# Kernel optimization log

Measured on AMD Instinct MI355X. Metric: run time of the kernel, lower is better.

Reference implementation:

```python
import jax, jax.numpy as jnp
from jax import lax
import numpy as np

B, N, NPOINTS, DOWN_NUM, K = 4, 4096, 4096, 1024, 16
EPS = 1e-5


def setup_inputs() -> dict:
    key = jax.random.key(0)
    ks = jax.random.split(key, 8)
    w = lambda k, s: jax.random.normal(k, s, jnp.float32) * 0.05
    return {
        "x": jax.random.normal(ks[0], (B, 3, N), jnp.float32),
        "w_in": w(ks[1], (8, 3)), "b_in": jnp.zeros((8,), jnp.float32),
        "w1": w(ks[2], (32, 16)), "g1w": jnp.ones((32,), jnp.float32), "g1b": jnp.zeros((32,), jnp.float32),
        "w2": w(ks[3], (64, 64)), "g2w": jnp.ones((64,), jnp.float32), "g2b": jnp.zeros((64,), jnp.float32),
        "w3": w(ks[4], (64, 128)), "g3w": jnp.ones((64,), jnp.float32), "g3b": jnp.zeros((64,), jnp.float32),
        "w4": w(ks[5], (128, 128)), "g4w": jnp.ones((128,), jnp.float32), "g4b": jnp.zeros((128,), jnp.float32),
    }


def _knn_idx(coor_k, coor_q, k):
    # coor_*: (B,3,N) -> idx (B,Nq,k) of k nearest points in coor_k for each query
    q = coor_q.transpose(0, 2, 1)  # (B,Nq,3)
    r = coor_k.transpose(0, 2, 1)  # (B,Nk,3)
    d = (jnp.sum(q * q, -1)[:, :, None] + jnp.sum(r * r, -1)[:, None, :]
         - 2.0 * jnp.einsum('bqc,bkc->bqk', q, r))
    _, idx = lax.top_k(-d, k)  # smallest distances
    return idx


def _graph_feature(coor_q, x_q, coor_k, x_k, k):
    # gather k-NN neighbor features and concat (neighbor - center, center)
    idx = _knn_idx(coor_k, coor_q, k)           # (B,Nq,k)
    xk = x_k.transpose(0, 2, 1)                  # (B,Nk,C)
    b, nq, _ = idx.shape
    c = xk.shape[-1]
    feat = jnp.take_along_axis(xk, idx.reshape(b, nq * k)[..., None], axis=1)
    feat = feat.reshape(b, nq, k, c).transpose(0, 3, 1, 2)  # (B,C,Nq,k)
    xq = x_q[:, :, :, None]                      # (B,C,Nq,1)
    return jnp.concatenate([feat - xq, jnp.broadcast_to(xq, feat.shape)], axis=1)


def _fps_idx(xyz, m):
    # furthest point sampling, xyz (B,N,3) -> idx (B,m); starts at point 0
    b, n, _ = xyz.shape
    def body(carry, _):
        dists, farthest = carry
        centroid = jnp.take_along_axis(xyz, farthest[:, None, None], axis=1)  # (B,1,3)
        d = jnp.sum((xyz - centroid) ** 2, axis=-1)
        dists = jnp.minimum(dists, d)
        return (dists, jnp.argmax(dists, axis=-1)), farthest
    init = (jnp.full((b, n), 1e10, xyz.dtype), jnp.zeros((b,), jnp.int32))
    _, idx = lax.scan(body, init, None, length=m)
    return idx.T  # (B,m)


def _fps_downsample(coor, f, m):
    idx = _fps_idx(coor.transpose(0, 2, 1), m)        # (B,m)
    combined = jnp.concatenate([coor, f], axis=1)      # (B,3+C,N)
    new = jnp.take_along_axis(combined, idx[:, None, :], axis=2)
    return new[:, :3], new[:, 3:]


def _group_norm(x, w, b, groups=4):
    bsz, c = x.shape[0], x.shape[1]
    xr = x.reshape(bsz, groups, -1)
    m = xr.mean(-1, keepdims=True)
    v = xr.var(-1, keepdims=True)
    xn = ((xr - m) * lax.rsqrt(v + EPS)).reshape(x.shape)
    shp = (1, c) + (1,) * (x.ndim - 2)
    return xn * w.reshape(shp) + b.reshape(shp)


def _block(f, w, gw, gb):
    # 1x1 conv (no bias) -> GroupNorm(4) -> LeakyReLU(0.2) -> max over neighbors
    h = jnp.einsum('oc,bcnk->bonk', w, f)
    h = jax.nn.leaky_relu(_group_norm(h, gw, gb), negative_slope=0.2)
    return h.max(axis=-1)


def reference(x, w_in, b_in, w1, g1w, g1b, w2, g2w, g2b, w3, g3w, g3b, w4, g4w, g4b):
    coor = x
    f = jnp.einsum('oc,bcn->bon', w_in, x) + b_in[None, :, None]
    inpc_f = f
    f = _graph_feature(coor, f, coor, f, K)
    f = _block(f, w1, g1w, g1b)                      # (B,32,N)
    coor_q, f_q = _fps_downsample(coor, f, NPOINTS // 2)
    f = _graph_feature(coor_q, f_q, coor, f, K)
    f = _block(f, w2, g2w, g2b)                      # (B,64,N/2)
    xyz1, point1 = coor_q, f
    coor = coor_q
    f = _graph_feature(coor, f, coor, f, K)
    f = _block(f, w3, g3w, g3b)                      # (B,64,N/2)
    coor_q, f_q = _fps_downsample(coor, f, DOWN_NUM)
    f = _graph_feature(coor_q, f_q, coor, f, K)
    f = _block(f, w4, g4w, g4b)                      # (B,128,DOWN_NUM)
    coor = coor_q
    return (coor, f, xyz1, point1, inpc_f)
```

## Files before the change

kernel.cpp:

```cpp
#include <hip/hip_runtime.h>
#include <float.h>
#include <math.h>

static constexpr int BATCH = 4;
static constexpr int NPT0  = 4096;

static constexpr size_t OFF_F0T  = 0;
static constexpr size_t OFF_F1T  = 524288;
static constexpr size_t OFF_FQ1T = 2621440;
static constexpr size_t OFF_F2T  = 3670016;
static constexpr size_t OFF_F3T  = 5767168;
static constexpr size_t OFF_FQ2T = 7864320;
static constexpr size_t OFF_CQ1  = 8912896;
static constexpr size_t OFF_CQ2  = 9011200;
static constexpr size_t OFF_H    = 9060352;
static constexpr size_t OFF_IDX1 = 42614784;
static constexpr size_t OFF_IDX2 = 43663360;
static constexpr size_t OFF_IDX3 = 44187648;
static constexpr size_t OFF_IDX4 = 44711936;
static constexpr size_t OFF_FPS1 = 44974080;
static constexpr size_t OFF_FPS2 = 45006848;
static constexpr size_t OFF_WD1  = 45023232;
static constexpr size_t OFF_WD2  = 45024256;
static constexpr size_t OFF_WD3  = 45032448;
static constexpr size_t OFF_WD4  = 45048832;
static constexpr size_t OFF_STAT = 45081600;
static constexpr size_t OFF_AB   = 45082624;
static constexpr size_t OFF_PART  = 45099008;
static constexpr size_t OFF_PART2 = OFF_PART;
static constexpr size_t OFF_PART3 = OFF_PART + 8388608;
static constexpr size_t OFF_PART4 = OFF_PART + 12582912;

static constexpr size_t OUT_COOR = 0;
static constexpr size_t OUT_F    = 12288;
static constexpr size_t OUT_XYZ1 = 536576;
static constexpr size_t OUT_PT1  = 561152;
static constexpr size_t OUT_INPC = 1085440;

__global__ __launch_bounds__(256) void k_prep(
    const float* __restrict__ w1, const float* __restrict__ w2,
    const float* __restrict__ w3, const float* __restrict__ w4,
    float* __restrict__ wd1, float* __restrict__ wd2,
    float* __restrict__ wd3, float* __restrict__ wd4,
    double* __restrict__ stats)
{
  int t = blockIdx.x * 256 + threadIdx.x;
  if (t < 128) stats[t] = 0.0;
  if (t < 32 * 8)   { int o = t / 8,  c = t % 8;  wd1[t] = w1[o*16  + 8   + c] - w1[o*16  + c]; }
  if (t < 64 * 32)  { int o = t / 32, c = t % 32; wd2[t] = w2[o*64  + 32  + c] - w2[o*64  + c]; }
  if (t < 64 * 64)  { int o = t / 64, c = t % 64; wd3[t] = w3[o*128 + 64  + c] - w3[o*128 + c]; }
  if (t < 128 * 64) { int o = t / 64, c = t % 64; wd4[t] = w4[o*128 + 64  + c] - w4[o*128 + c]; }
}

__global__ __launch_bounds__(256) void k_linear_in(
    const float* __restrict__ x, const float* __restrict__ w_in,
    const float* __restrict__ b_in, float* __restrict__ f0t,
    float* __restrict__ out_inpc)
{
  int t = blockIdx.x * 256 + threadIdx.x;
  int n = t & (NPT0 - 1);
  int b = t >> 12;
  float x0 = x[(size_t)b*3*NPT0 + n];
  float x1 = x[(size_t)b*3*NPT0 + NPT0 + n];
  float x2 = x[(size_t)b*3*NPT0 + 2*NPT0 + n];
#pragma unroll
  for (int o = 0; o < 8; ++o) {
    float v = __fmul_rn(w_in[o*3], x0);
    v = fmaf(w_in[o*3+1], x1, v);
    v = fmaf(w_in[o*3+2], x2, v);
    v = __fadd_rn(v, b_in[o]);
    f0t[(size_t)t * 8 + o] = v;
    out_inpc[((size_t)b*8 + o)*NPT0 + n] = v;
  }
}

__device__ __forceinline__ void knnp_dev(
    int vb, const float* __restrict__ cq, const float* __restrict__ ck,
    unsigned long long* __restrict__ part, int Nq, int Nk, int slices, void* smem)
{
  const int CS = 512;
  int s  = vb % slices;
  int r  = vb / slices;
  int qb = r % (Nq >> 8);
  int b  = r / (Nq >> 8);
  float4* cand = (float4*)smem;
  int t = threadIdx.x;
  const float* ckb = ck + (size_t)b*3*Nk;
  for (int jj = t; jj < CS; jj += 256) {
    int j = s*CS + jj;
    float xx = ckb[j], yy = ckb[Nk + j], zz = ckb[2*Nk + j];
    float sq = __fadd_rn(__fadd_rn(__fmul_rn(xx,xx), __fmul_rn(yy,yy)), __fmul_rn(zz,zz));
    cand[jj] = make_float4(xx, yy, zz, sq);
  }
  __syncthreads();
  int q = qb*256 + t;
  const float* cqb = cq + (size_t)b*3*Nq;
  float qx = cqb[q], qy = cqb[Nq + q], qz = cqb[2*Nq + q];
  float sqq = __fadd_rn(__fadd_rn(__fmul_rn(qx,qx), __fmul_rn(qy,qy)), __fmul_rn(qz,qz));

  unsigned long long bd[16];
#pragma unroll
  for (int sl = 0; sl < 16; ++sl) bd[sl] = ~0ull;
  unsigned long long wk = ~0ull; int ws = 0;

  for (int jj = 0; jj < CS; ++jj) {
    float4 c = cand[jj];
    float dot = __fmul_rn(c.x, qx);
    dot = fmaf(c.y, qy, dot);
    dot = fmaf(c.z, qz, dot);
    float d = __fsub_rn(__fadd_rn(sqq, c.w), __fmul_rn(2.0f, dot));
    unsigned u = __float_as_uint(d);
    u ^= (0x80000000u | (unsigned)((int)u >> 31));
    unsigned long long key = ((unsigned long long)u << 32) | (unsigned)(s*CS + jj);
    if (key < wk) {
      unsigned long long nw = 0; int nws = 0;
#pragma unroll
      for (int sl = 0; sl < 16; ++sl) {
        bool rep = (sl == ws);
        unsigned long long v = rep ? key : bd[sl];
        bd[sl] = v;
        bool g = v > nw;
        nw = g ? v : nw; nws = g ? sl : nws;
      }
      wk = nw; ws = nws;
    }
  }
  unsigned long long* op = part + (((size_t)b*Nq + q)*(size_t)slices + s)*16;
#pragma unroll
  for (int sl = 0; sl < 16; ++sl) op[sl] = bd[sl];
}

__global__ __launch_bounds__(256) void k_knnp(
    const float* __restrict__ cq, const float* __restrict__ ck,
    unsigned long long* __restrict__ part, int Nq, int Nk, int slices)
{
  extern __shared__ char smem[];
  knnp_dev(blockIdx.x, cq, ck, part, Nq, Nk, slices, smem);
}

__global__ __launch_bounds__(256) void k_merge(
    const unsigned long long* __restrict__ part, int* __restrict__ idx, int slices)
{
  int t = blockIdx.x * 256 + threadIdx.x;
  const unsigned long long* ip = part + (size_t)t * slices * 16;
  unsigned long long bd[16];
#pragma unroll
  for (int sl = 0; sl < 16; ++sl) bd[sl] = ~0ull;
  unsigned long long wk = ~0ull; int ws = 0;
  int n = slices * 16;
  for (int i = 0; i < n; ++i) {
    unsigned long long key = ip[i];
    if (key < wk) {
      unsigned long long nw = 0; int nws = 0;
#pragma unroll
      for (int sl = 0; sl < 16; ++sl) {
        bool rep = (sl == ws);
        unsigned long long v = rep ? key : bd[sl];
        bd[sl] = v;
        bool g = v > nw;
        nw = g ? v : nw; nws = g ? sl : nws;
      }
      wk = nw; ws = nws;
    }
  }
  int* op = idx + (size_t)t * 16;
#pragma unroll
  for (int sl = 0; sl < 16; ++sl) op[sl] = (int)(bd[sl] & 0xFFFFFFFFull);
}

template<int NN, int PPT>
__device__ __forceinline__ void fps_dev(
    int b, const float* __restrict__ coor, int m, int* __restrict__ fidx_all,
    float* __restrict__ ca_all, float* __restrict__ co_all, void* smem)
{
  float* sx = (float*)smem;
  float* sy = sx + NN;
  float* sz = sy + NN;
  unsigned long long* part = (unsigned long long*)(sz + NN);
  int t = threadIdx.x, lane = t & 63, wv = t >> 6;
  const float* cb = coor + (size_t)b*3*NN;
  float px[PPT], py[PPT], pz[PPT], pd[PPT];
#pragma unroll
  for (int i = 0; i < PPT; ++i) {
    int j = i*256 + t;
    px[i] = cb[j]; py[i] = cb[NN + j]; pz[i] = cb[2*NN + j];
    pd[i] = 1e10f;
    sx[j] = px[i]; sy[j] = py[i]; sz[j] = pz[i];
  }
  __syncthreads();
  float cx = sx[0], cy = sy[0], cz = sz[0];
  int* fidx = fidx_all + b*m;
  float* ca = ca_all + (size_t)b*3*m;
  float* co = co_all + (size_t)b*3*m;
  int cur = 0, par = 0;
  for (int it = 0; it < m; ++it) {
    if (t == 0) {
      fidx[it] = cur;
      ca[it] = cx; ca[m + it] = cy; ca[2*m + it] = cz;
      co[it] = cx; co[m + it] = cy; co[2*m + it] = cz;
    }
    unsigned long long kk[PPT];
#pragma unroll
    for (int i = 0; i < PPT; ++i) {
      float dx = __fsub_rn(px[i], cx);
      float dy = __fsub_rn(py[i], cy);
      float dz = __fsub_rn(pz[i], cz);
      float d = __fadd_rn(__fadd_rn(__fmul_rn(dx,dx), __fmul_rn(dy,dy)), __fmul_rn(dz,dz));
      float nd = fminf(pd[i], d);
      pd[i] = nd;
      kk[i] = ((unsigned long long)__float_as_uint(nd) << 32) | (unsigned)(~(i*256 + t));
    }
#pragma unroll
    for (int st = PPT/2; st >= 1; st >>= 1)
#pragma unroll
      for (int i = 0; i < st; ++i)
        if (kk[i + st] > kk[i]) kk[i] = kk[i + st];
    unsigned long long bk = kk[0];
#pragma unroll
    for (int mm = 1; mm < 64; mm <<= 1) {
      unsigned long long o = __shfl_xor(bk, mm, 64);
      bk = o > bk ? o : bk;
    }
    if (lane == 0) part[par*4 + wv] = bk;
    __syncthreads();
    unsigned long long k0 = part[par*4 + 0], k1 = part[par*4 + 1];
    unsigned long long k2 = part[par*4 + 2], k3 = part[par*4 + 3];
    k0 = k1 > k0 ? k1 : k0;
    k2 = k3 > k2 ? k3 : k2;
    k0 = k2 > k0 ? k2 : k0;
    cur = (int)(~(unsigned)(k0 & 0xFFFFFFFFull));
    cx = sx[cur]; cy = sy[cur]; cz = sz[cur];
    par ^= 1;
  }
}

template<int C, int COUT, int OC>
__device__ __forceinline__ void passA_dev(
    int vb, const float* __restrict__ xq, const float* __restrict__ xk,
    const int* __restrict__ idx, const float* __restrict__ w,
    const float* __restrict__ wdl, float* __restrict__ h,
    double* __restrict__ stats, int Nq, int Nk, void* smem)
{
  constexpr int NCH = COUT / OC;
  constexpr int GS  = COUT / 4;
  float* sxq   = (float*)smem;
  float* sbase = sxq + 16*C;
  int qb = Nq >> 4;
  int b = vb / qb, nb = vb % qb;
  int n0 = nb << 4;
  int t = threadIdx.x;
  for (int i = t; i < 16*C; i += 256) {
    int nn = i / C, cc = i % C;
    sxq[nn*C + cc] = xq[((size_t)b*Nq + n0 + nn)*C + cc];
  }
  __syncthreads();
  for (int i = t; i < 16*COUT; i += 256) {
    int nn = i / COUT, o = i % COUT;
    float acc = 0.f;
#pragma unroll 4
    for (int c = 0; c < C; ++c) acc = fmaf(wdl[o*C + c], sxq[nn*C + c], acc);
    sbase[nn*(COUT+1) + o] = acc;
  }
  __syncthreads();
  int lane = t & 63;
  int n_loc = t >> 4, kk = t & 15;
  int kidx = idx[((size_t)b*Nq + n0 + n_loc)*16 + kk];
  const float* xr = xk + ((size_t)b*Nk + kidx)*C;
  float* hrow = h + (((size_t)b*Nq + n0 + n_loc)*16 + kk)*(size_t)COUT;
#pragma unroll 1
  for (int oc = 0; oc < NCH; ++oc) {
    int o0 = oc * OC;
    float acc[OC];
#pragma unroll
    for (int oi = 0; oi < OC; ++oi) acc[oi] = sbase[n_loc*(COUT+1) + o0 + oi];
#pragma unroll 1
    for (int c4 = 0; c4 < C/4; ++c4) {
      float4 v = *(const float4*)(xr + c4*4);
#pragma unroll
      for (int oi = 0; oi < OC; ++oi) {
        const float* wr = w + (size_t)(o0 + oi)*(2*C) + c4*4;
        acc[oi] = fmaf(wr[0], v.x, acc[oi]);
        acc[oi] = fmaf(wr[1], v.y, acc[oi]);
        acc[oi] = fmaf(wr[2], v.z, acc[oi]);
        acc[oi] = fmaf(wr[3], v.w, acc[oi]);
      }
    }
#pragma unroll
    for (int oi = 0; oi < OC; ++oi) hrow[o0 + oi] = acc[oi];
    double s = 0.0, s2 = 0.0;
#pragma unroll
    for (int oi = 0; oi < OC; ++oi) { double dv = (double)acc[oi]; s += dv; s2 += dv*dv; }
#pragma unroll
    for (int mm = 1; mm < 64; mm <<= 1) {
      s  += __shfl_xor(s,  mm, 64);
      s2 += __shfl_xor(s2, mm, 64);
    }
    if (lane == 0) {
      int g = o0 / GS;
      atomicAdd(&stats[((size_t)b*4 + g)*2],     s);
      atomicAdd(&stats[((size_t)b*4 + g)*2 + 1], s2);
    }
  }
}

template<int C, int COUT, int OC>
__global__ __launch_bounds__(256) void k_passA(
    const float* __restrict__ xq, const float* __restrict__ xk,
    const int* __restrict__ idx, const float* __restrict__ w,
    const float* __restrict__ wdl, float* __restrict__ h,
    double* __restrict__ stats, int Nq, int Nk)
{
  extern __shared__ char smem[];
  passA_dev<C,COUT,OC>(blockIdx.x, xq, xk, idx, w, wdl, h, stats, Nq, Nk, smem);
}

__global__ __launch_bounds__(256) void k_megaA(
    const float* __restrict__ x, int* __restrict__ fps1,
    float* __restrict__ cq1, float* __restrict__ outXyz1,
    unsigned long long* __restrict__ part1)
{
  extern __shared__ char smem[];
  int vb = blockIdx.x;
  if (vb < 4) fps_dev<4096,16>(vb, x, 2048, fps1, cq1, outXyz1, smem);
  else        knnp_dev(vb - 4, x, x, part1, 4096, 4096, 8, smem);
}

__global__ __launch_bounds__(256) void k_megaB(
    const float* __restrict__ cq1, const float* __restrict__ x,
    int* __restrict__ fps2, float* __restrict__ cq2, float* __restrict__ outCoor,
    unsigned long long* __restrict__ part2, unsigned long long* __restrict__ part3,
    const float* __restrict__ f0t, const int* __restrict__ idx1,
    const float* __restrict__ w1, const float* __restrict__ wd1,
    float* __restrict__ h, double* __restrict__ st1)
{
  extern __shared__ char smem[];
  int vb = blockIdx.x;
  if      (vb < 4)            fps_dev<2048,8>(vb, cq1, 1024, fps2, cq2, outCoor, smem);
  else if (vb < 4 + 256)      knnp_dev(vb - 4,   cq1, x,   part2, 2048, 4096, 8, smem);
  else if (vb < 4 + 256+128)  knnp_dev(vb - 260, cq1, cq1, part3, 2048, 2048, 4, smem);
  else                        passA_dev<8,32,8>(vb - 388, f0t, f0t, idx1, w1, wd1,
                                                h, st1, 4096, 4096, smem);
}

__global__ void k_finalize(const double* __restrict__ stats,
                           const float* __restrict__ gw, const float* __restrict__ gb,
                           float* __restrict__ Ac, float* __restrict__ Bc,
                           int COUT, int Nq)
{
  int t = blockIdx.x * blockDim.x + threadIdx.x;
  if (t >= BATCH * COUT) return;
  int o = t % COUT, b = t / COUT;
  int GS = COUT / 4, g = o / GS;
  double cnt = (double)GS * (double)Nq * 16.0;
  double su = stats[((size_t)b*4 + g)*2];
  double s2 = stats[((size_t)b*4 + g)*2 + 1];
  double mean = su / cnt;
  double var = s2 / cnt - mean * mean;
  float vf = (float)var; if (vf < 0.f) vf = 0.f;
  float inv = 1.0f / sqrtf(vf + 1e-5f);
  float A = gw[o] * inv;
  Ac[b*COUT + o] = A;
  Bc[b*COUT + o] = gb[o] - (float)mean * A;
}

__global__ __launch_bounds__(256) void k_passB(
    const float* __restrict__ h, const float* __restrict__ Ac,
    const float* __restrict__ Bc, float* __restrict__ ft,
    float* __restrict__ ocn, int Nq, int COUT)
{
  int t = blockIdx.x * 256 + threadIdx.x;
  int o = t % COUT;
  int r = t / COUT;
  int n = r % Nq;
  int b = r / Nq;
  float A = Ac[b*COUT + o], Bb = Bc[b*COUT + o];
  const float* hp = h + (((size_t)b*Nq + n)*16)*(size_t)COUT + o;
  float m = -FLT_MAX;
#pragma unroll
  for (int k = 0; k < 16; ++k) {
    float v = hp[(size_t)k*COUT];
    float y = fmaf(v, A, Bb);
    y = (y >= 0.f) ? y : 0.2f*y;
    m = fmaxf(m, y);
  }
  if (ft)  ft[((size_t)b*Nq + n)*COUT + o] = m;
  if (ocn) ocn[((size_t)b*COUT + o)*Nq + n] = m;
}

__global__ __launch_bounds__(256) void k_gather_rows(
    const float* __restrict__ src, const int* __restrict__ fidx,
    float* __restrict__ dst, int M, int Cc, int Nsrc)
{
  int t = blockIdx.x * 256 + threadIdx.x;
  int cv = Cc >> 2;
  int c4 = t % cv;
  int r = t / cv;
  int i = r % M, b = r / M;
  int s = fidx[b*M + i];
  float4 v = *(const float4*)(src + ((size_t)b*Nsrc + s)*Cc + c4*4);
  *(float4*)(dst + ((size_t)b*M + i)*Cc + c4*4) = v;
}

extern "C" void kernel_launch(void* const* d_in, const int* in_sizes, int n_in,
                              void* d_out, int out_size, void* d_ws, size_t ws_size,
                              hipStream_t stream)
{
  (void)in_sizes; (void)n_in; (void)out_size; (void)ws_size;
  const float* x    = (const float*)d_in[0];
  const float* w_in = (const float*)d_in[1];
  const float* b_in = (const float*)d_in[2];
  const float* w1   = (const float*)d_in[3];
  const float* g1w  = (const float*)d_in[4];
  const float* g1b  = (const float*)d_in[5];
  const float* w2   = (const float*)d_in[6];
  const float* g2w  = (const float*)d_in[7];
  const float* g2b  = (const float*)d_in[8];
  const float* w3   = (const float*)d_in[9];
  const float* g3w  = (const float*)d_in[10];
  const float* g3b  = (const float*)d_in[11];
  const float* w4   = (const float*)d_in[12];
  const float* g4w  = (const float*)d_in[13];
  const float* g4b  = (const float*)d_in[14];
  float* out = (float*)d_out;
  char*  wsb = (char*)d_ws;

  float* f0t  = (float*)(wsb + OFF_F0T);
  float* f1t  = (float*)(wsb + OFF_F1T);
  float* fq1t = (float*)(wsb + OFF_FQ1T);
  float* f2t  = (float*)(wsb + OFF_F2T);
  float* f3t  = (float*)(wsb + OFF_F3T);
  float* fq2t = (float*)(wsb + OFF_FQ2T);
  float* cq1  = (float*)(wsb + OFF_CQ1);
  float* cq2  = (float*)(wsb + OFF_CQ2);
  float* h    = (float*)(wsb + OFF_H);
  int*   idx1 = (int*)(wsb + OFF_IDX1);
  int*   idx2 = (int*)(wsb + OFF_IDX2);
  int*   idx3 = (int*)(wsb + OFF_IDX3);
  int*   idx4 = (int*)(wsb + OFF_IDX4);
  int*   fps1 = (int*)(wsb + OFF_FPS1);
  int*   fps2 = (int*)(wsb + OFF_FPS2);
  float* wd1  = (float*)(wsb + OFF_WD1);
  float* wd2  = (float*)(wsb + OFF_WD2);
  float* wd3  = (float*)(wsb + OFF_WD3);
  float* wd4  = (float*)(wsb + OFF_WD4);
  double* statAll = (double*)(wsb + OFF_STAT);
  double* st1 = statAll, *st2 = statAll + 32, *st3 = statAll + 64, *st4 = statAll + 96;
  float* AB = (float*)(wsb + OFF_AB);
  float *A1 = AB,        *B1 = AB + 512;
  float *A2 = AB + 1024, *B2 = AB + 1536;
  float *A3 = AB + 2048, *B3 = AB + 2560;
  float *A4 = AB + 3072, *B4 = AB + 3584;
  unsigned long long* part1 = (unsigned long long*)(wsb + OFF_PART);
  unsigned long long* part2 = (unsigned long long*)(wsb + OFF_PART2);
  unsigned long long* part3 = (unsigned long long*)(wsb + OFF_PART3);
  unsigned long long* part4 = (unsigned long long*)(wsb + OFF_PART4);

  float* outCoor = out + OUT_COOR;
  float* outF    = out + OUT_F;
  float* outXyz1 = out + OUT_XYZ1;
  float* outPt1  = out + OUT_PT1;
  float* outInpc = out + OUT_INPC;

  k_prep<<<32, 256, 0, stream>>>(w1, w2, w3, w4, wd1, wd2, wd3, wd4, statAll);
  k_linear_in<<<64, 256, 0, stream>>>(x, w_in, b_in, f0t, outInpc);

  k_megaA<<<4 + 512, 256, 49216, stream>>>(x, fps1, cq1, outXyz1, part1);
  k_merge<<<64, 256, 0, stream>>>(part1, idx1, 8);

  k_megaB<<<4 + 256 + 128 + 1024, 256, 24640, stream>>>(
      cq1, x, fps2, cq2, outCoor, part2, part3, f0t, idx1, w1, wd1, h, st1);

  k_finalize<<<1, 256, 0, stream>>>(st1, g1w, g1b, A1, B1, 32, 4096);
  k_passB<<<2048, 256, 0, stream>>>(h, A1, B1, f1t, nullptr, 4096, 32);
  k_gather_rows<<<256, 256, 0, stream>>>(f1t, fps1, fq1t, 2048, 32, 4096);
  k_merge<<<32, 256, 0, stream>>>(part2, idx2, 8);
  k_merge<<<32, 256, 0, stream>>>(part3, idx3, 4);
  k_knnp<<<64, 256, 8192, stream>>>(cq2, cq1, part4, 1024, 2048, 4);
  k_merge<<<16, 256, 0, stream>>>(part4, idx4, 4);

  k_passA<32,64,16><<<512, 256, 6208, stream>>>(fq1t, f1t, idx2, w2, wd2, h, st2, 2048, 4096);
  k_finalize<<<1, 256, 0, stream>>>(st2, g2w, g2b, A2, B2, 64, 2048);
  k_passB<<<2048, 256, 0, stream>>>(h, A2, B2, f2t, outPt1, 2048, 64);

  k_passA<64,64,16><<<512, 256, 8256, stream>>>(f2t, f2t, idx3, w3, wd3, h, st3, 2048, 2048);
  k_finalize<<<1, 256, 0, stream>>>(st3, g3w, g3b, A3, B3, 64, 2048);
  k_passB<<<2048, 256, 0, stream>>>(h, A3, B3, f3t, nullptr, 2048, 64);

  k_gather_rows<<<256, 256, 0, stream>>>(f3t, fps2, fq2t, 1024, 64, 2048);
  k_passA<64,128,16><<<256, 256, 12352, stream>>>(fq2t, f3t, idx4, w4, wd4, h, st4, 1024, 2048);
  k_finalize<<<2, 256, 0, stream>>>(st4, g4w, g4b, A4, B4, 128, 1024);
  k_passB<<<2048, 256, 0, stream>>>(h, A4, B4, nullptr, outF, 1024, 128);
}
```

Baseline: 3.655 ms.

## Merge independent launches into mega-kernels and fold finalize/gather into consumers

```diff
diff --git a/kernel.cpp b/kernel.cpp
--- a/kernel.cpp
+++ b/kernel.cpp
@@ -7,10 +7,8 @@
 
 static constexpr size_t OFF_F0T  = 0;
 static constexpr size_t OFF_F1T  = 524288;
-static constexpr size_t OFF_FQ1T = 2621440;
 static constexpr size_t OFF_F2T  = 3670016;
 static constexpr size_t OFF_F3T  = 5767168;
-static constexpr size_t OFF_FQ2T = 7864320;
 static constexpr size_t OFF_CQ1  = 8912896;
 static constexpr size_t OFF_CQ2  = 9011200;
 static constexpr size_t OFF_H    = 9060352;
@@ -25,7 +23,6 @@
 static constexpr size_t OFF_WD3  = 45032448;
 static constexpr size_t OFF_WD4  = 45048832;
 static constexpr size_t OFF_STAT = 45081600;
-static constexpr size_t OFF_AB   = 45082624;
 static constexpr size_t OFF_PART  = 45099008;
 static constexpr size_t OFF_PART2 = OFF_PART;
 static constexpr size_t OFF_PART3 = OFF_PART + 8388608;
@@ -37,14 +34,14 @@
 static constexpr size_t OUT_PT1  = 561152;
 static constexpr size_t OUT_INPC = 1085440;
 
-__global__ __launch_bounds__(256) void k_prep(
-    const float* __restrict__ w1, const float* __restrict__ w2,
+__device__ __forceinline__ void prep_dev(
+    int vb, const float* __restrict__ w1, const float* __restrict__ w2,
     const float* __restrict__ w3, const float* __restrict__ w4,
     float* __restrict__ wd1, float* __restrict__ wd2,
     float* __restrict__ wd3, float* __restrict__ wd4,
     double* __restrict__ stats)
 {
-  int t = blockIdx.x * 256 + threadIdx.x;
+  int t = vb * 256 + threadIdx.x;
   if (t < 128) stats[t] = 0.0;
   if (t < 32 * 8)   { int o = t / 8,  c = t % 8;  wd1[t] = w1[o*16  + 8   + c] - w1[o*16  + c]; }
   if (t < 64 * 32)  { int o = t / 32, c = t % 32; wd2[t] = w2[o*64  + 32  + c] - w2[o*64  + c]; }
@@ -52,12 +49,12 @@
   if (t < 128 * 64) { int o = t / 64, c = t % 64; wd4[t] = w4[o*128 + 64  + c] - w4[o*128 + c]; }
 }
 
-__global__ __launch_bounds__(256) void k_linear_in(
-    const float* __restrict__ x, const float* __restrict__ w_in,
+__device__ __forceinline__ void linear_dev(
+    int vb, const float* __restrict__ x, const float* __restrict__ w_in,
     const float* __restrict__ b_in, float* __restrict__ f0t,
     float* __restrict__ out_inpc)
 {
-  int t = blockIdx.x * 256 + threadIdx.x;
+  int t = vb * 256 + threadIdx.x;
   int n = t & (NPT0 - 1);
   int b = t >> 12;
   float x0 = x[(size_t)b*3*NPT0 + n];
@@ -130,18 +127,11 @@
   for (int sl = 0; sl < 16; ++sl) op[sl] = bd[sl];
 }
 
-__global__ __launch_bounds__(256) void k_knnp(
-    const float* __restrict__ cq, const float* __restrict__ ck,
-    unsigned long long* __restrict__ part, int Nq, int Nk, int slices)
-{
-  extern __shared__ char smem[];
-  knnp_dev(blockIdx.x, cq, ck, part, Nq, Nk, slices, smem);
-}
-
-__global__ __launch_bounds__(256) void k_merge(
-    const unsigned long long* __restrict__ part, int* __restrict__ idx, int slices)
-{
-  int t = blockIdx.x * 256 + threadIdx.x;
+__device__ __forceinline__ void merge_dev(
+    int vb, const unsigned long long* __restrict__ part, int* __restrict__ idx,
+    int slices)
+{
+  int t = vb * 256 + threadIdx.x;
   const unsigned long long* ip = part + (size_t)t * slices * 16;
   unsigned long long bd[16];
 #pragma unroll
@@ -168,11 +158,18 @@
   for (int sl = 0; sl < 16; ++sl) op[sl] = (int)(bd[sl] & 0xFFFFFFFFull);
 }
 
+__global__ __launch_bounds__(256) void k_merge(
+    const unsigned long long* __restrict__ part, int* __restrict__ idx, int slices)
+{
+  merge_dev(blockIdx.x, part, idx, slices);
+}
+
 template<int NN, int PPT>
 __device__ __forceinline__ void fps_dev(
     int b, const float* __restrict__ coor, int m, int* __restrict__ fidx_all,
     float* __restrict__ ca_all, float* __restrict__ co_all, void* smem)
 {
+  __builtin_amdgcn_s_setprio(3);
   float* sx = (float*)smem;
   float* sy = sx + NN;
   float* sz = sy + NN;
@@ -180,11 +177,13 @@
   int t = threadIdx.x, lane = t & 63, wv = t >> 6;
   const float* cb = coor + (size_t)b*3*NN;
   float px[PPT], py[PPT], pz[PPT], pd[PPT];
+  unsigned invj[PPT];
 #pragma unroll
   for (int i = 0; i < PPT; ++i) {
     int j = i*256 + t;
     px[i] = cb[j]; py[i] = cb[NN + j]; pz[i] = cb[2*NN + j];
     pd[i] = 1e10f;
+    invj[i] = (unsigned)(~j);
     sx[j] = px[i]; sy[j] = py[i]; sz[j] = pz[i];
   }
   __syncthreads();
@@ -208,7 +207,7 @@
       float d = __fadd_rn(__fadd_rn(__fmul_rn(dx,dx), __fmul_rn(dy,dy)), __fmul_rn(dz,dz));
       float nd = fminf(pd[i], d);
       pd[i] = nd;
-      kk[i] = ((unsigned long long)__float_as_uint(nd) << 32) | (unsigned)(~(i*256 + t));
+      kk[i] = ((unsigned long long)__float_as_uint(nd) << 32) | invj[i];
     }
 #pragma unroll
     for (int st = PPT/2; st >= 1; st >>= 1)
@@ -223,10 +222,10 @@
     }
     if (lane == 0) part[par*4 + wv] = bk;
     __syncthreads();
-    unsigned long long k0 = part[par*4 + 0], k1 = part[par*4 + 1];
-    unsigned long long k2 = part[par*4 + 2], k3 = part[par*4 + 3];
-    k0 = k1 > k0 ? k1 : k0;
-    k2 = k3 > k2 ? k3 : k2;
+    ulonglong2 p01 = *(ulonglong2*)&part[par*4 + 0];
+    ulonglong2 p23 = *(ulonglong2*)&part[par*4 + 2];
+    unsigned long long k0 = p01.x > p01.y ? p01.x : p01.y;
+    unsigned long long k2 = p23.x > p23.y ? p23.x : p23.y;
     k0 = k2 > k0 ? k2 : k0;
     cur = (int)(~(unsigned)(k0 & 0xFFFFFFFFull));
     cx = sx[cur]; cy = sy[cur]; cz = sz[cur];
@@ -239,7 +238,8 @@
     int vb, const float* __restrict__ xq, const float* __restrict__ xk,
     const int* __restrict__ idx, const float* __restrict__ w,
     const float* __restrict__ wdl, float* __restrict__ h,
-    double* __restrict__ stats, int Nq, int Nk, void* smem)
+    double* __restrict__ stats, int Nq, int Nk,
+    const int* __restrict__ qmap, int NqSrc, void* smem)
 {
   constexpr int NCH = COUT / OC;
   constexpr int GS  = COUT / 4;
@@ -251,7 +251,8 @@
   int t = threadIdx.x;
   for (int i = t; i < 16*C; i += 256) {
     int nn = i / C, cc = i % C;
-    sxq[nn*C + cc] = xq[((size_t)b*Nq + n0 + nn)*C + cc];
+    int qrow = qmap ? qmap[b*Nq + n0 + nn] : (n0 + nn);
+    sxq[nn*C + cc] = xq[((size_t)b*NqSrc + qrow)*C + cc];
   }
   __syncthreads();
   for (int i = t; i < 16*COUT; i += 256) {
@@ -308,48 +309,24 @@
     const float* __restrict__ xq, const float* __restrict__ xk,
     const int* __restrict__ idx, const float* __restrict__ w,
     const float* __restrict__ wdl, float* __restrict__ h,
-    double* __restrict__ stats, int Nq, int Nk)
+    double* __restrict__ stats, int Nq, int Nk,
+    const int* __restrict__ qmap, int NqSrc)
 {
   extern __shared__ char smem[];
-  passA_dev<C,COUT,OC>(blockIdx.x, xq, xk, idx, w, wdl, h, stats, Nq, Nk, smem);
-}
-
-__global__ __launch_bounds__(256) void k_megaA(
-    const float* __restrict__ x, int* __restrict__ fps1,
-    float* __restrict__ cq1, float* __restrict__ outXyz1,
-    unsigned long long* __restrict__ part1)
-{
-  extern __shared__ char smem[];
-  int vb = blockIdx.x;
-  if (vb < 4) fps_dev<4096,16>(vb, x, 2048, fps1, cq1, outXyz1, smem);
-  else        knnp_dev(vb - 4, x, x, part1, 4096, 4096, 8, smem);
-}
-
-__global__ __launch_bounds__(256) void k_megaB(
-    const float* __restrict__ cq1, const float* __restrict__ x,
-    int* __restrict__ fps2, float* __restrict__ cq2, float* __restrict__ outCoor,
-    unsigned long long* __restrict__ part2, unsigned long long* __restrict__ part3,
-    const float* __restrict__ f0t, const int* __restrict__ idx1,
-    const float* __restrict__ w1, const float* __restrict__ wd1,
-    float* __restrict__ h, double* __restrict__ st1)
-{
-  extern __shared__ char smem[];
-  int vb = blockIdx.x;
-  if      (vb < 4)            fps_dev<2048,8>(vb, cq1, 1024, fps2, cq2, outCoor, smem);
-  else if (vb < 4 + 256)      knnp_dev(vb - 4,   cq1, x,   part2, 2048, 4096, 8, smem);
-  else if (vb < 4 + 256+128)  knnp_dev(vb - 260, cq1, cq1, part3, 2048, 2048, 4, smem);
-  else                        passA_dev<8,32,8>(vb - 388, f0t, f0t, idx1, w1, wd1,
-                                                h, st1, 4096, 4096, smem);
-}
-
-__global__ void k_finalize(const double* __restrict__ stats,
-                           const float* __restrict__ gw, const float* __restrict__ gb,
-                           float* __restrict__ Ac, float* __restrict__ Bc,
-                           int COUT, int Nq)
-{
-  int t = blockIdx.x * blockDim.x + threadIdx.x;
-  if (t >= BATCH * COUT) return;
-  int o = t % COUT, b = t / COUT;
+  passA_dev<C,COUT,OC>(blockIdx.x, xq, xk, idx, w, wdl, h, stats, Nq, Nk,
+                       qmap, NqSrc, smem);
+}
+
+__device__ __forceinline__ void passB_dev(
+    int vb, const float* __restrict__ h, const double* __restrict__ stats,
+    const float* __restrict__ gw, const float* __restrict__ gb,
+    float* __restrict__ ft, float* __restrict__ ocn, int Nq, int COUT)
+{
+  int t = vb * 256 + threadIdx.x;
+  int o = t % COUT;
+  int r = t / COUT;
+  int n = r % Nq;
+  int b = r / Nq;
   int GS = COUT / 4, g = o / GS;
   double cnt = (double)GS * (double)Nq * 16.0;
   double su = stats[((size_t)b*4 + g)*2];
@@ -359,21 +336,7 @@
   float vf = (float)var; if (vf < 0.f) vf = 0.f;
   float inv = 1.0f / sqrtf(vf + 1e-5f);
   float A = gw[o] * inv;
-  Ac[b*COUT + o] = A;
-  Bc[b*COUT + o] = gb[o] - (float)mean * A;
-}
-
-__global__ __launch_bounds__(256) void k_passB(
-    const float* __restrict__ h, const float* __restrict__ Ac,
-    const float* __restrict__ Bc, float* __restrict__ ft,
-    float* __restrict__ ocn, int Nq, int COUT)
-{
-  int t = blockIdx.x * 256 + threadIdx.x;
-  int o = t % COUT;
-  int r = t / COUT;
-  int n = r % Nq;
-  int b = r / Nq;
-  float A = Ac[b*COUT + o], Bb = Bc[b*COUT + o];
+  float Bb = gb[o] - (float)mean * A;
   const float* hp = h + (((size_t)b*Nq + n)*16)*(size_t)COUT + o;
   float m = -FLT_MAX;
 #pragma unroll
@@ -387,18 +350,80 @@
   if (ocn) ocn[((size_t)b*COUT + o)*Nq + n] = m;
 }
 
-__global__ __launch_bounds__(256) void k_gather_rows(
-    const float* __restrict__ src, const int* __restrict__ fidx,
-    float* __restrict__ dst, int M, int Cc, int Nsrc)
-{
-  int t = blockIdx.x * 256 + threadIdx.x;
-  int cv = Cc >> 2;
-  int c4 = t % cv;
-  int r = t / cv;
-  int i = r % M, b = r / M;
-  int s = fidx[b*M + i];
-  float4 v = *(const float4*)(src + ((size_t)b*Nsrc + s)*Cc + c4*4);
-  *(float4*)(dst + ((size_t)b*M + i)*Cc + c4*4) = v;
+__global__ __launch_bounds__(256) void k_passB(
+    const float* __restrict__ h, const double* __restrict__ stats,
+    const float* __restrict__ gw, const float* __restrict__ gb,
+    float* __restrict__ ft, float* __restrict__ ocn, int Nq, int COUT)
+{
+  passB_dev(blockIdx.x, h, stats, gw, gb, ft, ocn, Nq, COUT);
+}
+
+__global__ __launch_bounds__(256) void k_megaA(
+    const float* __restrict__ x, const float* __restrict__ w_in,
+    const float* __restrict__ b_in, float* __restrict__ f0t,
+    float* __restrict__ outInpc,
+    const float* __restrict__ w1, const float* __restrict__ w2,
+    const float* __restrict__ w3, const float* __restrict__ w4,
+    float* __restrict__ wd1, float* __restrict__ wd2,
+    float* __restrict__ wd3, float* __restrict__ wd4,
+    double* __restrict__ stats,
+    int* __restrict__ fps1, float* __restrict__ cq1, float* __restrict__ outXyz1,
+    unsigned long long* __restrict__ part1)
+{
+  extern __shared__ char smem[];
+  int vb = blockIdx.x;
+  if      (vb < 4)   fps_dev<4096,16>(vb, x, 2048, fps1, cq1, outXyz1, smem);
+  else if (vb < 36)  prep_dev(vb - 4, w1, w2, w3, w4, wd1, wd2, wd3, wd4, stats);
+  else if (vb < 100) linear_dev(vb - 36, x, w_in, b_in, f0t, outInpc);
+  else               knnp_dev(vb - 100, x, x, part1, 4096, 4096, 8, smem);
+}
+
+__global__ __launch_bounds__(256) void k_megaB(
+    const float* __restrict__ cq1, const float* __restrict__ x,
+    int* __restrict__ fps2, float* __restrict__ cq2, float* __restrict__ outCoor,
+    unsigned long long* __restrict__ part2, unsigned long long* __restrict__ part3,
+    const float* __restrict__ f0t, const int* __restrict__ idx1,
+    const float* __restrict__ w1, const float* __restrict__ wd1,
+    float* __restrict__ h, double* __restrict__ st1)
+{
+  extern __shared__ char smem[];
+  int vb = blockIdx.x;
+  if      (vb < 4)           fps_dev<2048,8>(vb, cq1, 1024, fps2, cq2, outCoor, smem);
+  else if (vb < 4 + 256)     knnp_dev(vb - 4,   cq1, x,   part2, 2048, 4096, 8, smem);
+  else if (vb < 4 + 256+128) knnp_dev(vb - 260, cq1, cq1, part3, 2048, 2048, 4, smem);
+  else                       passA_dev<8,32,8>(vb - 388, f0t, f0t, idx1, w1, wd1,
+                                               h, st1, 4096, 4096, nullptr, 4096, smem);
+}
+
+__global__ __launch_bounds__(256) void k_megaC(
+    const float* __restrict__ cq2, const float* __restrict__ cq1,
+    unsigned long long* __restrict__ part4,
+    const unsigned long long* __restrict__ part2, int* __restrict__ idx2,
+    const unsigned long long* __restrict__ part3, int* __restrict__ idx3,
+    const float* __restrict__ h, const double* __restrict__ st1,
+    const float* __restrict__ g1w, const float* __restrict__ g1b,
+    float* __restrict__ f1t)
+{
+  extern __shared__ char smem[];
+  int vb = blockIdx.x;
+  if      (vb < 64)  knnp_dev(vb, cq2, cq1, part4, 1024, 2048, 4, smem);
+  else if (vb < 96)  merge_dev(vb - 64, part2, idx2, 8);
+  else if (vb < 128) merge_dev(vb - 96, part3, idx3, 4);
+  else               passB_dev(vb - 128, h, st1, g1w, g1b, f1t, nullptr, 4096, 32);
+}
+
+__global__ __launch_bounds__(256) void k_megaD(
+    const unsigned long long* __restrict__ part4, int* __restrict__ idx4,
+    const float* __restrict__ f1t, const int* __restrict__ idx2,
+    const float* __restrict__ w2, const float* __restrict__ wd2,
+    float* __restrict__ h, double* __restrict__ st2,
+    const int* __restrict__ fps1)
+{
+  extern __shared__ char smem[];
+  int vb = blockIdx.x;
+  if (vb < 16) merge_dev(vb, part4, idx4, 4);
+  else         passA_dev<32,64,16>(vb - 16, f1t, f1t, idx2, w2, wd2, h, st2,
+                                   2048, 4096, fps1, 4096, smem);
 }
 
 extern "C" void kernel_launch(void* const* d_in, const int* in_sizes, int n_in,
@@ -426,10 +451,8 @@
 
   float* f0t  = (float*)(wsb + OFF_F0T);
   float* f1t  = (float*)(wsb + OFF_F1T);
-  float* fq1t = (float*)(wsb + OFF_FQ1T);
   float* f2t  = (float*)(wsb + OFF_F2T);
   float* f3t  = (float*)(wsb + OFF_F3T);
-  float* fq2t = (float*)(wsb + OFF_FQ2T);
   float* cq1  = (float*)(wsb + OFF_CQ1);
   float* cq2  = (float*)(wsb + OFF_CQ2);
   float* h    = (float*)(wsb + OFF_H);
@@ -445,11 +468,6 @@
   float* wd4  = (float*)(wsb + OFF_WD4);
   double* statAll = (double*)(wsb + OFF_STAT);
   double* st1 = statAll, *st2 = statAll + 32, *st3 = statAll + 64, *st4 = statAll + 96;
-  float* AB = (float*)(wsb + OFF_AB);
-  float *A1 = AB,        *B1 = AB + 512;
-  float *A2 = AB + 1024, *B2 = AB + 1536;
-  float *A3 = AB + 2048, *B3 = AB + 2560;
-  float *A4 = AB + 3072, *B4 = AB + 3584;
   unsigned long long* part1 = (unsigned long long*)(wsb + OFF_PART);
   unsigned long long* part2 = (unsigned long long*)(wsb + OFF_PART2);
   unsigned long long* part3 = (unsigned long long*)(wsb + OFF_PART3);
@@ -461,33 +479,23 @@
   float* outPt1  = out + OUT_PT1;
   float* outInpc = out + OUT_INPC;
 
-  k_prep<<<32, 256, 0, stream>>>(w1, w2, w3, w4, wd1, wd2, wd3, wd4, statAll);
-  k_linear_in<<<64, 256, 0, stream>>>(x, w_in, b_in, f0t, outInpc);
-
-  k_megaA<<<4 + 512, 256, 49216, stream>>>(x, fps1, cq1, outXyz1, part1);
+  k_megaA<<<612, 256, 49216, stream>>>(x, w_in, b_in, f0t, outInpc,
+      w1, w2, w3, w4, wd1, wd2, wd3, wd4, statAll, fps1, cq1, outXyz1, part1);
   k_merge<<<64, 256, 0, stream>>>(part1, idx1, 8);
 
-  k_megaB<<<4 + 256 + 128 + 1024, 256, 24640, stream>>>(
+  k_megaB<<<1412, 256, 24640, stream>>>(
       cq1, x, fps2, cq2, outCoor, part2, part3, f0t, idx1, w1, wd1, h, st1);
 
-  k_finalize<<<1, 256, 0, stream>>>(st1, g1w, g1b, A1, B1, 32, 4096);
-  k_passB<<<2048, 256, 0, stream>>>(h, A1, B1, f1t, nullptr, 4096, 32);
-  k_gather_rows<<<256, 256, 0, stream>>>(f1t, fps1, fq1t, 2048, 32, 4096);
-  k_merge<<<32, 256, 0, stream>>>(part2, idx2, 8);
-  k_merge<<<32, 256, 0, stream>>>(part3, idx3, 4);
-  k_knnp<<<64, 256, 8192, stream>>>(cq2, cq1, part4, 1024, 2048, 4);
-  k_merge<<<16, 256, 0, stream>>>(part4, idx4, 4);
-
-  k_passA<32,64,16><<<512, 256, 6208, stream>>>(fq1t, f1t, idx2, w2, wd2, h, st2, 2048, 4096);
-  k_finalize<<<1, 256, 0, stream>>>(st2, g2w, g2b, A2, B2, 64, 2048);
-  k_passB<<<2048, 256, 0, stream>>>(h, A2, B2, f2t, outPt1, 2048, 64);
-
-  k_passA<64,64,16><<<512, 256, 8256, stream>>>(f2t, f2t, idx3, w3, wd3, h, st3, 2048, 2048);
-  k_finalize<<<1, 256, 0, stream>>>(st3, g3w, g3b, A3, B3, 64, 2048);
-  k_passB<<<2048, 256, 0, stream>>>(h, A3, B3, f3t, nullptr, 2048, 64);
-
-  k_gather_rows<<<256, 256, 0, stream>>>(f3t, fps2, fq2t, 1024, 64, 2048);
-  k_passA<64,128,16><<<256, 256, 12352, stream>>>(fq2t, f3t, idx4, w4, wd4, h, st4, 1024, 2048);
-  k_finalize<<<2, 256, 0, stream>>>(st4, g4w, g4b, A4, B4, 128, 1024);
-  k_passB<<<2048, 256, 0, stream>>>(h, A4, B4, nullptr, outF, 1024, 128);
-}
+  k_megaC<<<2176, 256, 8192, stream>>>(
+      cq2, cq1, part4, part2, idx2, part3, idx3, h, st1, g1w, g1b, f1t);
+
+  k_megaD<<<528, 256, 6208, stream>>>(part4, idx4, f1t, idx2, w2, wd2, h, st2, fps1);
+
+  k_passB<<<2048, 256, 0, stream>>>(h, st2, g2w, g2b, f2t, outPt1, 2048, 64);
+  k_passA<64,64,16><<<512, 256, 8256, stream>>>(f2t, f2t, idx3, w3, wd3, h, st3,
+                                                2048, 2048, nullptr, 2048);
+  k_passB<<<2048, 256, 0, stream>>>(h, st3, g3w, g3b, f3t, nullptr, 2048, 64);
+  k_passA<64,128,16><<<256, 256, 12352, stream>>>(f3t, f3t, idx4, w4, wd4, h, st4,
+                                                  1024, 2048, fps2, 2048);
+  k_passB<<<2048, 256, 0, stream>>>(h, st4, g4w, g4b, nullptr, outF, 1024, 128);
+}
```

New measurement: 3.397 ms. 1.08x faster.
